# Performance work log

Measured on AMD Instinct MI355X. Metric: run time of the kernel, lower is better.

## Reference

```python
import jax, jax.numpy as jnp
import numpy as np


def conv1x1(x, w, b):
    # x: [B, C, H, W], w: [O, C], b: [O] -> [B, O, H, W]
    return jnp.einsum('bchw,oc->bohw', x, w) + b[None, :, None, None]


def setup_inputs() -> dict:
    key = jax.random.key(0)
    ks = jax.random.split(key, 9)
    B, C, H, W = 2, 64, 96, 96
    inter = C // 2
    s = 0.05
    return {
        'x': jax.random.normal(ks[0], (B, C, H, W), dtype=jnp.float32),
        'g_w': jax.random.normal(ks[1], (inter, C), dtype=jnp.float32) * s,
        'g_b': jax.random.normal(ks[2], (inter,), dtype=jnp.float32) * s,
        'theta_w': jax.random.normal(ks[3], (inter, C), dtype=jnp.float32) * s,
        'theta_b': jax.random.normal(ks[4], (inter,), dtype=jnp.float32) * s,
        'phi_w': jax.random.normal(ks[5], (inter, C), dtype=jnp.float32) * s,
        'phi_b': jax.random.normal(ks[6], (inter,), dtype=jnp.float32) * s,
        'W_w': jax.random.normal(ks[7], (C, inter), dtype=jnp.float32) * s,
        'W_b': jax.random.normal(ks[8], (C,), dtype=jnp.float32) * s,
    }


def reference(x, g_w, g_b, theta_w, theta_b, phi_w, phi_b, W_w, W_b):
    B, C, H, W = x.shape
    inter = g_w.shape[0]
    N = H * W
    g_x = conv1x1(x, g_w, g_b).reshape(B, inter, N)          # [B, inter, N]
    theta_x = conv1x1(x, theta_w, theta_b).reshape(B, inter, N)  # [B, inter, N]
    phi_x = conv1x1(x, phi_w, phi_b).reshape(B, inter, N)    # [B, inter, N]
    # f[b, n, m] = sum_i phi[b, i, n] * theta[b, i, m]  -> [B, N, N]
    f = jnp.einsum('bin,bim->bnm', phi_x, theta_x)
    f_div_C = jax.nn.softmax(f, axis=-1)
    # y[b, n, i] = sum_m f_div_C[b, n, m] * g_x[b, i, m]
    y = jnp.einsum('bnm,bim->bni', f_div_C, g_x)             # [B, N, inter]
    y = jnp.transpose(y, (0, 2, 1)).reshape(B, inter, H, W)
    W_y = conv1x1(y, W_w, W_b)
    return W_y + x
```

## Files before the change

### kernel.cpp

```cpp
#include <hip/hip_runtime.h>
#include <cstdint>

#define BN 9216
#define NB 2
#define CIN 64
#define DI 32
#define MC 8
#define NCHUNK 288
#define LOG2E 1.4426950408889634f

typedef __attribute__((ext_vector_type(4))) float f32x4;
typedef __attribute__((ext_vector_type(8))) __bf16 bf16x8;
typedef __attribute__((ext_vector_type(4))) __bf16 bf16x4;
typedef __attribute__((ext_vector_type(4))) short s16x4;
typedef __attribute__((ext_vector_type(4))) unsigned int u32x4;

__device__ __forceinline__ unsigned short f2bf(float f) {
    unsigned int u = __builtin_bit_cast(unsigned int, f);
    u += 0x7FFFu + ((u >> 16) & 1u);
    return (unsigned short)(u >> 16);
}
__device__ __forceinline__ unsigned int packbf(float lo, float hi) {
    return (unsigned int)f2bf(lo) | ((unsigned int)f2bf(hi) << 16);
}

__device__ __forceinline__ float exp2_hw(float x) {
    float r;
    asm("v_exp_f32 %0, %1" : "=v"(r) : "v"(x));
    return r;
}

__device__ __forceinline__ f32x4 mfma16(bf16x4 a, bf16x4 b, f32x4 c) {
#if __has_builtin(__builtin_amdgcn_mfma_f32_16x16x16bf16_1k)
    return __builtin_amdgcn_mfma_f32_16x16x16bf16_1k(
        __builtin_bit_cast(s16x4, a), __builtin_bit_cast(s16x4, b), c, 0, 0, 0);
#elif __has_builtin(__builtin_amdgcn_mfma_f32_16x16x16_bf16)
    return __builtin_amdgcn_mfma_f32_16x16x16_bf16(a, b, c, 0, 0, 0);
#else
    f32x4 d;
    asm("v_mfma_f32_16x16x16_bf16 %0, %1, %2, %3"
        : "=v"(d) : "v"(a), "v"(b), "v"(c));
    return d;
#endif
}

__global__ __launch_bounds__(64) void qkv_kernel(
    const float* __restrict__ x,
    const float* __restrict__ g_w, const float* __restrict__ g_b,
    const float* __restrict__ th_w, const float* __restrict__ th_b,
    const float* __restrict__ ph_w, const float* __restrict__ ph_b,
    unsigned short* __restrict__ qT, unsigned short* __restrict__ kT,
    unsigned short* __restrict__ vv)
{
    __shared__ float wsh[3 * 8 * CIN];
    __shared__ float bsh[3 * 8];
    const int og = blockIdx.y;
    const int b = blockIdx.z;
    const int tid = threadIdx.x;
    for (int i = tid; i < 8 * CIN; i += 64) {
        const int o = i / CIN, c = i % CIN;
        wsh[0 * 512 + i] = ph_w[(size_t)(og * 8 + o) * CIN + c] * LOG2E;
        wsh[1 * 512 + i] = th_w[(size_t)(og * 8 + o) * CIN + c];
        wsh[2 * 512 + i] = g_w [(size_t)(og * 8 + o) * CIN + c];
    }
    if (tid < 8) {
        bsh[tid]      = ph_b[og * 8 + tid] * LOG2E;
        bsh[8 + tid]  = th_b[og * 8 + tid];
        bsh[16 + tid] = g_b [og * 8 + tid];
    }
    __syncthreads();

    const int n = blockIdx.x * 64 + tid;
    const float* xp = x + (size_t)b * CIN * BN + n;

    float aq[8], ak[8], av[8];
#pragma unroll
    for (int o = 0; o < 8; ++o) {
        aq[o] = bsh[o]; ak[o] = bsh[8 + o]; av[o] = bsh[16 + o];
    }
    for (int c0 = 0; c0 < CIN; c0 += 16) {
        float xv[16];
#pragma unroll
        for (int u = 0; u < 16; ++u) xv[u] = xp[(size_t)(c0 + u) * BN];
#pragma unroll
        for (int u = 0; u < 16; ++u) {
#pragma unroll
            for (int o = 0; o < 8; ++o) {
                aq[o] += wsh[0 * 512 + o * CIN + c0 + u] * xv[u];
                ak[o] += wsh[1 * 512 + o * CIN + c0 + u] * xv[u];
                av[o] += wsh[2 * 512 + o * CIN + c0 + u] * xv[u];
            }
        }
    }

    {
        unsigned short* qp = qT + ((size_t)b * BN + n) * DI + og * 8;
        u32x4 tq = {packbf(aq[0], aq[1]), packbf(aq[2], aq[3]),
                    packbf(aq[4], aq[5]), packbf(aq[6], aq[7])};
        *(u32x4*)qp = tq;
        unsigned short* kp = kT + ((size_t)b * BN + n) * DI + og * 8;
        u32x4 tk = {packbf(ak[0], ak[1]), packbf(ak[2], ak[3]),
                    packbf(ak[4], ak[5]), packbf(ak[6], ak[7])};
        *(u32x4*)kp = tk;
    }
    {
        const int r = n & 31;
        const int pos = (n & ~31) + ((r >> 2) & 3) * 8 + (r >> 4) * 4 + (r & 3);
        unsigned short* vp = vv + (size_t)b * DI * BN + pos;
#pragma unroll
        for (int o = 0; o < 8; ++o) vp[(size_t)(og * 8 + o) * BN] = f2bf(av[o]);
    }
}

__global__ __launch_bounds__(256) void attn_partial(
    const unsigned short* __restrict__ qT, const unsigned short* __restrict__ kT,
    const unsigned short* __restrict__ vv,
    float* __restrict__ pacc, float* __restrict__ pl)
{
    __shared__ float red_l[4][2][16];
    __shared__ float red_acc[4][2][512];

    const int b  = blockIdx.z;
    const int mc = blockIdx.y;
    const int nc = blockIdx.x;
    const int n0 = nc * 32;
    const int tid = threadIdx.x;
    const int w = tid >> 6;
    const int lane = tid & 63;
    const int h = lane >> 4;
    const int q = lane & 15;

    const unsigned short* qTb = qT + (size_t)b * BN * DI;
    const unsigned short* kTb = kT + (size_t)b * BN * DI;
    const unsigned short* vb  = vv + (size_t)b * DI * BN;

    bf16x8 qfA = *(const bf16x8*)(qTb + ((size_t)(n0 + q)) * DI + 8 * h);
    bf16x8 qfB = *(const bf16x8*)(qTb + ((size_t)(n0 + 16 + q)) * DI + 8 * h);
    const f32x4 zero = {0.f, 0.f, 0.f, 0.f};
    f32x4 a0A = zero, a1A = zero, a0B = zero, a1B = zero;
    float lA = 0.f, lB = 0.f;

    const unsigned short* vrow0 = vb + (size_t)q * BN;
    const unsigned short* vrow1 = vb + (size_t)(16 + q) * BN;

    int m0 = mc * 1152 + w * 32;
#pragma unroll 1
    for (int it = 0; it < 9; ++it, m0 += 128) {
        bf16x8 k0 = *(const bf16x8*)(kTb + ((size_t)(m0 + q)) * DI + 8 * h);
        bf16x8 k1 = *(const bf16x8*)(kTb + ((size_t)(m0 + 16 + q)) * DI + 8 * h);
        bf16x8 vr0 = *(const bf16x8*)(vrow0 + m0 + 8 * h);
        bf16x8 vr1 = *(const bf16x8*)(vrow1 + m0 + 8 * h);
        f32x4 s0A = __builtin_amdgcn_mfma_f32_16x16x32_bf16(k0, qfA, zero, 0, 0, 0);
        f32x4 s1A = __builtin_amdgcn_mfma_f32_16x16x32_bf16(k1, qfA, zero, 0, 0, 0);
        f32x4 s0B = __builtin_amdgcn_mfma_f32_16x16x32_bf16(k0, qfB, zero, 0, 0, 0);
        f32x4 s1B = __builtin_amdgcn_mfma_f32_16x16x32_bf16(k1, qfB, zero, 0, 0, 0);

        bf16x4 vlo0 = __builtin_shufflevector(vr0, vr0, 0, 1, 2, 3);
        bf16x4 vhi0 = __builtin_shufflevector(vr0, vr0, 4, 5, 6, 7);
        bf16x4 vlo1 = __builtin_shufflevector(vr1, vr1, 0, 1, 2, 3);
        bf16x4 vhi1 = __builtin_shufflevector(vr1, vr1, 4, 5, 6, 7);

        {
            float p0 = exp2_hw(s0A[0]), p1 = exp2_hw(s0A[1]);
            float p2 = exp2_hw(s0A[2]), p3 = exp2_hw(s0A[3]);
            float p4 = exp2_hw(s1A[0]), p5 = exp2_hw(s1A[1]);
            float p6 = exp2_hw(s1A[2]), p7 = exp2_hw(s1A[3]);
            lA += ((p0 + p1) + (p2 + p3)) + ((p4 + p5) + (p6 + p7));
            bf16x4 pf0 = {(__bf16)p0, (__bf16)p1, (__bf16)p2, (__bf16)p3};
            bf16x4 pf1 = {(__bf16)p4, (__bf16)p5, (__bf16)p6, (__bf16)p7};
            a0A = mfma16(vlo0, pf0, a0A);
            a0A = mfma16(vhi0, pf1, a0A);
            a1A = mfma16(vlo1, pf0, a1A);
            a1A = mfma16(vhi1, pf1, a1A);
        }
        {
            float p0 = exp2_hw(s0B[0]), p1 = exp2_hw(s0B[1]);
            float p2 = exp2_hw(s0B[2]), p3 = exp2_hw(s0B[3]);
            float p4 = exp2_hw(s1B[0]), p5 = exp2_hw(s1B[1]);
            float p6 = exp2_hw(s1B[2]), p7 = exp2_hw(s1B[3]);
            lB += ((p0 + p1) + (p2 + p3)) + ((p4 + p5) + (p6 + p7));
            bf16x4 pf0 = {(__bf16)p0, (__bf16)p1, (__bf16)p2, (__bf16)p3};
            bf16x4 pf1 = {(__bf16)p4, (__bf16)p5, (__bf16)p6, (__bf16)p7};
            a0B = mfma16(vlo0, pf0, a0B);
            a0B = mfma16(vhi0, pf1, a0B);
            a1B = mfma16(vlo1, pf0, a1B);
            a1B = mfma16(vhi1, pf1, a1B);
        }
    }

    lA += __shfl_xor(lA, 16, 64); lA += __shfl_xor(lA, 32, 64);
    lB += __shfl_xor(lB, 16, 64); lB += __shfl_xor(lB, 32, 64);

    if (lane < 16) { red_l[w][0][lane] = lA; red_l[w][1][lane] = lB; }

#pragma unroll
    for (int t = 0; t < 4; ++t) {
        red_acc[w][0][(4 * h + t) * 16 + q]      = a0A[t];
        red_acc[w][0][(16 + 4 * h + t) * 16 + q] = a1A[t];
        red_acc[w][1][(4 * h + t) * 16 + q]      = a0B[t];
        red_acc[w][1][(16 + 4 * h + t) * 16 + q] = a1B[t];
    }
    __syncthreads();

    {
        const int np = tid & 31;
        const int ig = tid >> 5;
        const int tt = np >> 4, qq = np & 15;
        const size_t pbase = (((size_t)b * MC + mc) * NCHUNK + nc) * 1024;
#pragma unroll
        for (int ii = 0; ii < 4; ++ii) {
            const int i = ig * 4 + ii;
            float ysum = red_acc[0][tt][i * 16 + qq] + red_acc[1][tt][i * 16 + qq]
                       + red_acc[2][tt][i * 16 + qq] + red_acc[3][tt][i * 16 + qq];
            pacc[pbase + (size_t)i * 32 + np] = ysum;
        }
        if (tid < 32) {
            float L = red_l[0][tt][qq] + red_l[1][tt][qq]
                    + red_l[2][tt][qq] + red_l[3][tt][qq];
            pl[(((size_t)b * MC + mc) * NCHUNK + nc) * 32 + np] = L;
        }
    }
}

__global__ __launch_bounds__(256) void combine_outconv(
    const float* __restrict__ pacc, const float* __restrict__ pl,
    const float* __restrict__ Ww, const float* __restrict__ Wb,
    const float* __restrict__ x, float* __restrict__ out)
{
    __shared__ float sl[MC * 32];
    __shared__ float ysh[32 * 33];
    __shared__ float WwT[32 * 65];
    __shared__ float swb[64];

    const int b  = blockIdx.y;
    const int nc = blockIdx.x;
    const int tid = threadIdx.x;
    const int n  = tid & 31;
    const int ig = tid >> 5;

    {
        sl[tid] = pl[(((size_t)b * MC + (tid >> 5)) * NCHUNK + nc) * 32 + (tid & 31)];
#pragma unroll
        for (int e = tid; e < 2048; e += 256)
            WwT[(e & 31) * 65 + (e >> 5)] = Ww[e];
        if (tid < 64) swb[tid] = Wb[tid];
    }

    float xr[8];
    const float* xp = x + ((size_t)b * CIN + ig * 8) * BN + nc * 32 + n;
#pragma unroll
    for (int oo = 0; oo < 8; ++oo) xr[oo] = xp[(size_t)oo * BN];

    __syncthreads();

    {
        float L = 0.f;
#pragma unroll
        for (int mc2 = 0; mc2 < MC; ++mc2) L += sl[mc2 * 32 + n];
        const float inv = 1.0f / L;

        const size_t pb0 = (((size_t)b * MC) * NCHUNK + nc) * 1024;
#pragma unroll
        for (int ii = 0; ii < 4; ++ii) {
            const int i = ig * 4 + ii;
            float y = 0.f;
#pragma unroll
            for (int mc2 = 0; mc2 < MC; ++mc2)
                y += pacc[pb0 + (size_t)mc2 * NCHUNK * 1024 + (size_t)i * 32 + n];
            ysh[i * 33 + n] = y * inv;
        }
    }
    __syncthreads();

    {
        float acc[8];
#pragma unroll
        for (int oo = 0; oo < 8; ++oo) acc[oo] = swb[ig * 8 + oo];
#pragma unroll
        for (int i = 0; i < 32; ++i) {
            float yv = ysh[i * 33 + n];
#pragma unroll
            for (int oo = 0; oo < 8; ++oo)
                acc[oo] += WwT[i * 65 + ig * 8 + oo] * yv;
        }
        float* op = out + ((size_t)b * CIN + ig * 8) * BN + nc * 32 + n;
#pragma unroll
        for (int oo = 0; oo < 8; ++oo) op[(size_t)oo * BN] = acc[oo] + xr[oo];
    }
}

extern "C" void kernel_launch(void* const* d_in, const int* in_sizes, int n_in,
                              void* d_out, int out_size, void* d_ws, size_t ws_size,
                              hipStream_t stream)
{
    const float* x    = (const float*)d_in[0];
    const float* g_w  = (const float*)d_in[1];
    const float* g_b  = (const float*)d_in[2];
    const float* th_w = (const float*)d_in[3];
    const float* th_b = (const float*)d_in[4];
    const float* ph_w = (const float*)d_in[5];
    const float* ph_b = (const float*)d_in[6];
    const float* W_w  = (const float*)d_in[7];
    const float* W_b  = (const float*)d_in[8];
    float* out = (float*)d_out;

    char* ws = (char*)d_ws;
    unsigned short* qT = (unsigned short*)(ws);
    unsigned short* kT = (unsigned short*)(ws + 1179648);
    unsigned short* vv = (unsigned short*)(ws + 2359296);
    float* pacc = (float*)(ws + 3538944);
    float* pl   = (float*)(ws + 22413312);

    dim3 g1(BN / 64, 4, NB);
    qkv_kernel<<<g1, 64, 0, stream>>>(x, g_w, g_b, th_w, th_b, ph_w, ph_b,
                                      qT, kT, vv);
    dim3 g2(NCHUNK, MC, NB);
    attn_partial<<<g2, 256, 0, stream>>>(qT, kT, vv, pacc, pl);
    dim3 g3(NCHUNK, NB);
    combine_outconv<<<g3, 256, 0, stream>>>(pacc, pl, W_w, W_b, x, out);
}
```

Before: 156.0 us.

## Use 16x16x32 MFMA for PV via permuted K rows and prefetch next tile

Rows of K are now loaded in a permuted order so the score fragment can feed a single 16x16x32 bf16 MFMA for the P·V product, replacing two 16x16x16 MFMAs. Because of this, V is stored in natural order and the interleaved write in the QKV kernel is dropped. The attention loop also software-prefetches the next K/V tile into registers before computing the current one. This is meant to halve the PV MFMA instruction count and hide global load latency, at the cost of extra live registers.

```diff
diff --git a/kernel.cpp b/kernel.cpp
--- a/kernel.cpp
+++ b/kernel.cpp
@@ -11,8 +11,6 @@
 
 typedef __attribute__((ext_vector_type(4))) float f32x4;
 typedef __attribute__((ext_vector_type(8))) __bf16 bf16x8;
-typedef __attribute__((ext_vector_type(4))) __bf16 bf16x4;
-typedef __attribute__((ext_vector_type(4))) short s16x4;
 typedef __attribute__((ext_vector_type(4))) unsigned int u32x4;
 
 __device__ __forceinline__ unsigned short f2bf(float f) {
@@ -28,20 +26,6 @@
     float r;
     asm("v_exp_f32 %0, %1" : "=v"(r) : "v"(x));
     return r;
-}
-
-__device__ __forceinline__ f32x4 mfma16(bf16x4 a, bf16x4 b, f32x4 c) {
-#if __has_builtin(__builtin_amdgcn_mfma_f32_16x16x16bf16_1k)
-    return __builtin_amdgcn_mfma_f32_16x16x16bf16_1k(
-        __builtin_bit_cast(s16x4, a), __builtin_bit_cast(s16x4, b), c, 0, 0, 0);
-#elif __has_builtin(__builtin_amdgcn_mfma_f32_16x16x16_bf16)
-    return __builtin_amdgcn_mfma_f32_16x16x16_bf16(a, b, c, 0, 0, 0);
-#else
-    f32x4 d;
-    asm("v_mfma_f32_16x16x16_bf16 %0, %1, %2, %3"
-        : "=v"(d) : "v"(a), "v"(b), "v"(c));
-    return d;
-#endif
 }
 
 __global__ __launch_bounds__(64) void qkv_kernel(
@@ -104,9 +88,7 @@
         *(u32x4*)kp = tk;
     }
     {
-        const int r = n & 31;
-        const int pos = (n & ~31) + ((r >> 2) & 3) * 8 + (r >> 4) * 4 + (r & 3);
-        unsigned short* vp = vv + (size_t)b * DI * BN + pos;
+        unsigned short* vp = vv + (size_t)b * DI * BN + n;
 #pragma unroll
         for (int o = 0; o < 8; ++o) vp[(size_t)(og * 8 + o) * BN] = f2bf(av[o]);
     }
@@ -129,6 +111,7 @@
     const int lane = tid & 63;
     const int h = lane >> 4;
     const int q = lane & 15;
+    const int sig = 8 * (q >> 2) + (q & 3);
 
     const unsigned short* qTb = qT + (size_t)b * BN * DI;
     const unsigned short* kTb = kT + (size_t)b * BN * DI;
@@ -140,38 +123,34 @@
     f32x4 a0A = zero, a1A = zero, a0B = zero, a1B = zero;
     float lA = 0.f, lB = 0.f;
 
-    const unsigned short* vrow0 = vb + (size_t)q * BN;
-    const unsigned short* vrow1 = vb + (size_t)(16 + q) * BN;
+    const unsigned short* krow = kTb + (size_t)sig * DI + 8 * h;
+    const unsigned short* vrow0 = vb + (size_t)q * BN + 8 * h;
+    const unsigned short* vrow1 = vb + (size_t)(16 + q) * BN + 8 * h;
 
     int m0 = mc * 1152 + w * 32;
-#pragma unroll 1
-    for (int it = 0; it < 9; ++it, m0 += 128) {
-        bf16x8 k0 = *(const bf16x8*)(kTb + ((size_t)(m0 + q)) * DI + 8 * h);
-        bf16x8 k1 = *(const bf16x8*)(kTb + ((size_t)(m0 + 16 + q)) * DI + 8 * h);
-        bf16x8 vr0 = *(const bf16x8*)(vrow0 + m0 + 8 * h);
-        bf16x8 vr1 = *(const bf16x8*)(vrow1 + m0 + 8 * h);
+
+#define LD_K0(m) (*(const bf16x8*)(krow + (size_t)(m) * DI))
+#define LD_K1(m) (*(const bf16x8*)(krow + (size_t)((m) + 4) * DI))
+#define LD_V0(m) (*(const bf16x8*)(vrow0 + (m)))
+#define LD_V1(m) (*(const bf16x8*)(vrow1 + (m)))
+
+    bf16x8 ck0 = LD_K0(m0), ck1 = LD_K1(m0), cv0 = LD_V0(m0), cv1 = LD_V1(m0);
+
+    auto compute = [&](bf16x8 k0, bf16x8 k1, bf16x8 v0, bf16x8 v1) {
         f32x4 s0A = __builtin_amdgcn_mfma_f32_16x16x32_bf16(k0, qfA, zero, 0, 0, 0);
         f32x4 s1A = __builtin_amdgcn_mfma_f32_16x16x32_bf16(k1, qfA, zero, 0, 0, 0);
         f32x4 s0B = __builtin_amdgcn_mfma_f32_16x16x32_bf16(k0, qfB, zero, 0, 0, 0);
         f32x4 s1B = __builtin_amdgcn_mfma_f32_16x16x32_bf16(k1, qfB, zero, 0, 0, 0);
-
-        bf16x4 vlo0 = __builtin_shufflevector(vr0, vr0, 0, 1, 2, 3);
-        bf16x4 vhi0 = __builtin_shufflevector(vr0, vr0, 4, 5, 6, 7);
-        bf16x4 vlo1 = __builtin_shufflevector(vr1, vr1, 0, 1, 2, 3);
-        bf16x4 vhi1 = __builtin_shufflevector(vr1, vr1, 4, 5, 6, 7);
-
         {
             float p0 = exp2_hw(s0A[0]), p1 = exp2_hw(s0A[1]);
             float p2 = exp2_hw(s0A[2]), p3 = exp2_hw(s0A[3]);
             float p4 = exp2_hw(s1A[0]), p5 = exp2_hw(s1A[1]);
             float p6 = exp2_hw(s1A[2]), p7 = exp2_hw(s1A[3]);
             lA += ((p0 + p1) + (p2 + p3)) + ((p4 + p5) + (p6 + p7));
-            bf16x4 pf0 = {(__bf16)p0, (__bf16)p1, (__bf16)p2, (__bf16)p3};
-            bf16x4 pf1 = {(__bf16)p4, (__bf16)p5, (__bf16)p6, (__bf16)p7};
-            a0A = mfma16(vlo0, pf0, a0A);
-            a0A = mfma16(vhi0, pf1, a0A);
-            a1A = mfma16(vlo1, pf0, a1A);
-            a1A = mfma16(vhi1, pf1, a1A);
+            bf16x8 pf = {(__bf16)p0, (__bf16)p1, (__bf16)p2, (__bf16)p3,
+                         (__bf16)p4, (__bf16)p5, (__bf16)p6, (__bf16)p7};
+            a0A = __builtin_amdgcn_mfma_f32_16x16x32_bf16(v0, pf, a0A, 0, 0, 0);
+            a1A = __builtin_amdgcn_mfma_f32_16x16x32_bf16(v1, pf, a1A, 0, 0, 0);
         }
         {
             float p0 = exp2_hw(s0B[0]), p1 = exp2_hw(s0B[1]);
@@ -179,14 +158,28 @@
             float p4 = exp2_hw(s1B[0]), p5 = exp2_hw(s1B[1]);
             float p6 = exp2_hw(s1B[2]), p7 = exp2_hw(s1B[3]);
             lB += ((p0 + p1) + (p2 + p3)) + ((p4 + p5) + (p6 + p7));
-            bf16x4 pf0 = {(__bf16)p0, (__bf16)p1, (__bf16)p2, (__bf16)p3};
-            bf16x4 pf1 = {(__bf16)p4, (__bf16)p5, (__bf16)p6, (__bf16)p7};
-            a0B = mfma16(vlo0, pf0, a0B);
-            a0B = mfma16(vhi0, pf1, a0B);
-            a1B = mfma16(vlo1, pf0, a1B);
-            a1B = mfma16(vhi1, pf1, a1B);
-        }
-    }
+            bf16x8 pf = {(__bf16)p0, (__bf16)p1, (__bf16)p2, (__bf16)p3,
+                         (__bf16)p4, (__bf16)p5, (__bf16)p6, (__bf16)p7};
+            a0B = __builtin_amdgcn_mfma_f32_16x16x32_bf16(v0, pf, a0B, 0, 0, 0);
+            a1B = __builtin_amdgcn_mfma_f32_16x16x32_bf16(v1, pf, a1B, 0, 0, 0);
+        }
+    };
+
+#pragma unroll 1
+    for (int it = 0; it < 8; ++it) {
+        const int mn = m0 + 128;
+        bf16x8 nk0 = LD_K0(mn), nk1 = LD_K1(mn);
+        bf16x8 nv0 = LD_V0(mn), nv1 = LD_V1(mn);
+        compute(ck0, ck1, cv0, cv1);
+        ck0 = nk0; ck1 = nk1; cv0 = nv0; cv1 = nv1;
+        m0 = mn;
+    }
+    compute(ck0, ck1, cv0, cv1);
+
+#undef LD_K0
+#undef LD_K1
+#undef LD_V0
+#undef LD_V1
 
     lA += __shfl_xor(lA, 16, 64); lA += __shfl_xor(lA, 32, 64);
     lB += __shfl_xor(lB, 16, 64); lB += __shfl_xor(lB, 32, 64);
```

New measurement: 154.2 us. No clear change (-1.2%).
